# Performance work log

Hardware: AMD Instinct MI355X
Metric: run time of the kernel (lower is better)

## Reference

```python
import jax, jax.numpy as jnp
import numpy as np

D_MODEL = 768
N_HEADS = 12
HEAD_DIM = D_MODEL // N_HEADS


def setup_inputs() -> dict:
    key = jax.random.key(0)
    ks = jax.random.split(key, 9)
    s = 1.0 / np.sqrt(D_MODEL)
    inp = {
        "inputs": jax.random.normal(ks[0], (1, 4096, D_MODEL), dtype=jnp.float32),
        "Wq": jax.random.uniform(ks[1], (D_MODEL, D_MODEL), jnp.float32, -s, s),
        "bq": jax.random.uniform(ks[2], (D_MODEL,), jnp.float32, -s, s),
        "Wk": jax.random.uniform(ks[3], (D_MODEL, D_MODEL), jnp.float32, -s, s),
        "bk": jax.random.uniform(ks[4], (D_MODEL,), jnp.float32, -s, s),
        "Wv": jax.random.uniform(ks[5], (D_MODEL, D_MODEL), jnp.float32, -s, s),
        "bv": jax.random.uniform(ks[6], (D_MODEL,), jnp.float32, -s, s),
        "Wo": jax.random.uniform(ks[7], (D_MODEL, D_MODEL), jnp.float32, -s, s),
        "bo": jax.random.uniform(ks[8], (D_MODEL,), jnp.float32, -s, s),
    }
    return inp


def reference(inputs, Wq, bq, Wk, bk, Wv, bv, Wo, bo):
    B, S, D = inputs.shape
    H, Hd = N_HEADS, HEAD_DIM

    def split_heads(x):  # [B,S,D] -> [B,H,S,Hd]
        return x.reshape(B, S, H, Hd).transpose(0, 2, 1, 3)

    # nn.Linear computes x @ W.T + b
    Q = split_heads(inputs @ Wq.T + bq)
    K = split_heads(inputs @ Wk.T + bk)
    V = split_heads(inputs @ Wv.T + bv)

    scores = jnp.einsum("bhsd,bhtd->bhst", Q, K) / jnp.sqrt(jnp.float32(Hd))
    causal = jnp.tril(jnp.ones((S, S), dtype=bool))  # True = keep
    scores = jnp.where(causal, scores, -jnp.inf)
    attn = jax.nn.softmax(scores, axis=-1)  # dropout is identity in eval

    out = jnp.einsum("bhst,bhtd->bhsd", attn, V)
    out = out.transpose(0, 2, 1, 3).reshape(B, S, D)
    return out @ Wo.T + bo
```

## Files before the change

### kernel.cpp

```cpp
#include <hip/hip_runtime.h>
#include <stdint.h>

#define SEQ 4096
#define DM 768
#define NH 12
#define HD 64

typedef unsigned short u16;
typedef short short8 __attribute__((ext_vector_type(8)));
typedef float floatx4 __attribute__((ext_vector_type(4)));
typedef float floatx16 __attribute__((ext_vector_type(16)));
typedef u16 u16x4 __attribute__((ext_vector_type(4)));

__device__ inline u16 f2b(float f) {
  union { float f; uint32_t u; } v; v.f = f;
  uint32_t u = v.u;
  return (u16)((u + 0x7fffu + ((u >> 16) & 1u)) >> 16);
}

__device__ inline float b2f(u16 x) {
  union { uint32_t u; float f; } v; v.u = ((uint32_t)x) << 16;
  return v.f;
}

#if defined(__has_builtin)
#if __has_builtin(__builtin_amdgcn_cvt_pk_bf16_f32)
#define HAVE_PK_BF16 1
#endif
#endif

__device__ inline uint32_t pk_bf16(float a, float b) {
#ifdef HAVE_PK_BF16
  typedef __bf16 bf16x2_t __attribute__((ext_vector_type(2)));
  union { bf16x2_t v; uint32_t u; } c;
  c.v = __builtin_amdgcn_cvt_pk_bf16_f32(a, b);
  return c.u;
#else
  uint32_t r;
  asm("v_cvt_pk_bf16_f32 %0, %1, %2" : "=v"(r) : "v"(a), "v"(b));
  return r;
#endif
}

__device__ inline void pl32swap(uint32_t& a, uint32_t& b) {
  asm("v_permlane32_swap_b32 %0, %1" : "+v"(a), "+v"(b));
}

__device__ inline void load_lds16(const void* g, void* l) {
  __builtin_amdgcn_global_load_lds(
      (const __attribute__((address_space(1))) uint32_t*)g,
      (__attribute__((address_space(3))) uint32_t*)l, 16, 0, 0);
}

__global__ __launch_bounds__(256) void convert_all(
    const float* __restrict__ X, const float* __restrict__ Wq,
    const float* __restrict__ Wk, const float* __restrict__ Wv,
    const float* __restrict__ Wo,
    u16* __restrict__ Xb, u16* __restrict__ Wqb, u16* __restrict__ Wkb,
    u16* __restrict__ Wvb, u16* __restrict__ Wob) {
  int t = blockIdx.x * 256 + threadIdx.x;
  const int NX = SEQ * DM / 4;
  const int NW = DM * DM / 4;
  const float* src; u16* dst; int off;
  if (t < NX)               { src = X;  dst = Xb;  off = t; }
  else if (t < NX + NW)     { src = Wq; dst = Wqb; off = t - NX; }
  else if (t < NX + 2 * NW) { src = Wk; dst = Wkb; off = t - NX - NW; }
  else if (t < NX + 3 * NW) { src = Wv; dst = Wvb; off = t - NX - 2 * NW; }
  else if (t < NX + 4 * NW) { src = Wo; dst = Wob; off = t - NX - 3 * NW; }
  else return;
  float4 v = *(const float4*)(src + (size_t)off * 4);
  uint2 o;
  o.x = pk_bf16(v.x, v.y);
  o.y = pk_bf16(v.z, v.w);
  *(uint2*)(dst + (size_t)off * 4) = o;
}

__global__ __launch_bounds__(256) void gemm_qkv(
    const u16* __restrict__ Xb,
    const u16* __restrict__ Wqb, const u16* __restrict__ Wkb,
    const u16* __restrict__ Wvb,
    const float* __restrict__ bq, const float* __restrict__ bk,
    const float* __restrict__ bv,
    u16* __restrict__ Qh, u16* __restrict__ Kh, u16* __restrict__ VtG) {
  const u16* W; const float* bias;
  const int z = blockIdx.z;
  if (z == 0)      { W = Wqb; bias = bq; }
  else if (z == 1) { W = Wkb; bias = bk; }
  else             { W = Wvb; bias = bv; }

  __shared__ u16 smem[16384];

  const int tid = threadIdx.x;
  const int wave = tid >> 6, lane = tid & 63;
  const int g = lane >> 4, ln = lane & 15;
  const int m0 = blockIdx.y * 64, n0 = blockIdx.x * 64;
  const int wm = (wave & 1) * 32, wn = (wave >> 1) * 32;
  const int srow = lane >> 3;
  const int schunk = (lane & 7) ^ srow;
  const int swz = ln & 7;

  floatx4 acc[2][2] = {};

#pragma unroll
  for (int i = 0; i < 2; ++i) {
    int u = wave * 2 + i;
    load_lds16(Xb + (size_t)(m0 + u * 8 + srow) * DM + schunk * 8, smem + u * 512);
    load_lds16(W + (size_t)(n0 + u * 8 + srow) * DM + schunk * 8,
               smem + 8192 + u * 512);
  }

  for (int kt = 0; kt < 12; ++kt) {
    const int cur = kt & 1;
    __syncthreads();
    if (kt < 11) {
      const int k0 = (kt + 1) * 64, nb = cur ^ 1;
#pragma unroll
      for (int i = 0; i < 2; ++i) {
        int u = wave * 2 + i;
        load_lds16(Xb + (size_t)(m0 + u * 8 + srow) * DM + k0 + schunk * 8,
                   smem + nb * 4096 + u * 512);
        load_lds16(W + (size_t)(n0 + u * 8 + srow) * DM + k0 + schunk * 8,
                   smem + 8192 + nb * 4096 + u * 512);
      }
    }
    const u16* Ac = smem + cur * 4096;
    const u16* Bc = smem + 8192 + cur * 4096;
    short8 af[2][2], bf[2][2];
#pragma unroll
    for (int mi = 0; mi < 2; ++mi)
#pragma unroll
      for (int kh = 0; kh < 2; ++kh)
        af[mi][kh] = *(const short8*)(Ac + (wm + mi * 16 + ln) * 64 +
                                      ((kh * 4 + g) ^ swz) * 8);
#pragma unroll
    for (int ni = 0; ni < 2; ++ni)
#pragma unroll
      for (int kh = 0; kh < 2; ++kh)
        bf[ni][kh] = *(const short8*)(Bc + (wn + ni * 16 + ln) * 64 +
                                      ((kh * 4 + g) ^ swz) * 8);
#pragma unroll
    for (int kh = 0; kh < 2; ++kh)
#pragma unroll
      for (int mi = 0; mi < 2; ++mi)
#pragma unroll
        for (int ni = 0; ni < 2; ++ni)
          acc[mi][ni] = __builtin_amdgcn_mfma_f32_16x16x32_bf16(
              af[mi][kh], bf[ni][kh], acc[mi][ni], 0, 0, 0);
  }

  const float qscale = 0.125f * 1.44269504089f;
  const int hh = n0 >> 6;
  __syncthreads();

  if (z == 2) {
#pragma unroll
    for (int mi = 0; mi < 2; ++mi) {
      int row0 = wm + mi * 16 + g * 4;
#pragma unroll
      for (int ni = 0; ni < 2; ++ni) {
        int col = wn + ni * 16 + ln;
        float b = bias[n0 + col];
        uint2 o;
        o.x = pk_bf16(acc[mi][ni][0] + b, acc[mi][ni][1] + b);
        o.y = pk_bf16(acc[mi][ni][2] + b, acc[mi][ni][3] + b);
        *(uint2*)(smem + col * 72 + row0) = o;
      }
    }
    __syncthreads();
#pragma unroll
    for (int t = 0; t < 2; ++t) {
      int unit = tid + t * 256;
      int dcol = unit >> 3, ch = unit & 7;
      short8 v = *(const short8*)(smem + dcol * 72 + ch * 8);
      *(short8*)(VtG + ((size_t)(hh * 64 + dcol)) * SEQ + m0 + ch * 8) = v;
    }
  } else {
    u16* out = (z == 0) ? Qh : Kh;
    float cs = (z == 0) ? qscale : 1.0f;
#pragma unroll
    for (int mi = 0; mi < 2; ++mi) {
      int row0 = wm + mi * 16 + g * 4;
#pragma unroll
      for (int ni = 0; ni < 2; ++ni) {
        int col = wn + ni * 16 + ln;
        float b = bias[n0 + col];
        uint32_t w0 = pk_bf16((acc[mi][ni][0] + b) * cs, (acc[mi][ni][1] + b) * cs);
        uint32_t w1 = pk_bf16((acc[mi][ni][2] + b) * cs, (acc[mi][ni][3] + b) * cs);
        smem[(row0 + 0) * 72 + col] = (u16)w0;
        smem[(row0 + 1) * 72 + col] = (u16)(w0 >> 16);
        smem[(row0 + 2) * 72 + col] = (u16)w1;
        smem[(row0 + 3) * 72 + col] = (u16)(w1 >> 16);
      }
    }
    __syncthreads();
#pragma unroll
    for (int t = 0; t < 2; ++t) {
      int unit = tid + t * 256;
      int row = unit >> 3, ch = unit & 7;
      short8 v = *(const short8*)(smem + row * 72 + ch * 8);
      *(short8*)(out + ((size_t)hh * SEQ + m0 + row) * HD + ch * 8) = v;
    }
  }
}

#define CHUNK 16
#define M0 40.0f
__global__ __launch_bounds__(256, 3) void attn_chunk(
    const u16* __restrict__ Qh, const u16* __restrict__ Kh,
    const u16* __restrict__ VtG, u16* __restrict__ Opart,
    float2* __restrict__ Mlp) {
  const int p = blockIdx.y * NH + blockIdx.x;
  const int slot = p % 24, cyc = p / 24;
  const int qq = 3 * (slot & 7) + (slot >> 3);
  const int h = qq >> 1;
  const int b = 79 - (cyc * 2 + (qq & 1));
  int qB, ci;
  if (b < 8)       { qB = b;               ci = 0; }
  else if (b < 24) { int r = b - 8;  qB = 8 + (r >> 1); ci = r & 1; }
  else if (b < 48) { int r = b - 24; int d = r / 3; qB = 16 + d; ci = r - d * 3; }
  else             { int r = b - 48; qB = 24 + (r >> 2); ci = r & 3; }
  const int kb0 = ci * CHUNK;
  const int kb1 = min(kb0 + CHUNK, 2 * qB + 2);

  const int tid = threadIdx.x, wave = tid >> 6, lane = tid & 63;
  const int hi = lane >> 5, lq = lane & 31;
  const int q0 = qB * 128;
  const int qwave = q0 + wave * 32;
  const int srow = lane >> 3;
  const int schunk = (lane & 7) ^ srow;
  const int rsw = lane & 7;

  __shared__ u16 Ks[3 * 4096];
  __shared__ u16 Vt[3 * 4096];

  const int qglob = qwave + lq;
  const u16* Qbase = Qh + ((size_t)h * SEQ + qglob) * HD;
  short8 aq[4];
#pragma unroll
  for (int s = 0; s < 4; ++s)
    aq[s] = *(const short8*)(Qbase + s * 16 + hi * 8);

  floatx16 oacc[2] = {};
  floatx4 lacc = {};

  const size_t kbase = (size_t)h * SEQ * HD;
  const size_t vbase = (size_t)h * 64 * SEQ;

  auto stage = [&](int kbIdx, int buf) {
#pragma unroll
    for (int i = 0; i < 2; ++i) {
      int u = wave * 2 + i;
      load_lds16(Kh + kbase + (size_t)(kbIdx * 64 + u * 8 + srow) * HD + schunk * 8,
                 Ks + buf * 4096 + u * 512);
      load_lds16(VtG + vbase + (size_t)(u * 8 + srow) * SEQ + kbIdx * 64 + schunk * 8,
                 Vt + buf * 4096 + u * 512);
    }
  };

  stage(kb0, 0);
  if (kb0 + 1 < kb1) stage(kb0 + 1, 1);

  for (int kb = kb0; kb < kb1; ++kb) {
    const int cur = (kb - kb0) % 3;
    if (kb + 1 < kb1) asm volatile("s_waitcnt vmcnt(4)" ::: "memory");
    else              asm volatile("s_waitcnt vmcnt(0)" ::: "memory");
    __builtin_amdgcn_s_barrier();
    if (kb + 2 < kb1) stage(kb + 2, (cur + 2) % 3);

    const u16* Kc = Ks + cur * 4096;
    const u16* Vc = Vt + cur * 4096;

    if (kb * 64 > qwave + 31) continue;

    floatx16 st[2];
#pragma unroll
    for (int kblk = 0; kblk < 2; ++kblk)
#pragma unroll
      for (int r = 0; r < 16; ++r) st[kblk][r] = -M0;
    __builtin_amdgcn_s_setprio(1);
#pragma unroll
    for (int s = 0; s < 4; ++s)
#pragma unroll
      for (int kblk = 0; kblk < 2; ++kblk) {
        short8 kf = *(const short8*)(Kc + (kblk * 32 + lq) * 64 +
                                     ((s * 2 + hi) ^ rsw) * 8);
        st[kblk] = __builtin_amdgcn_mfma_f32_32x32x16_bf16(kf, aq[s], st[kblk],
                                                           0, 0, 0);
      }
    __builtin_amdgcn_s_setprio(0);

    if (kb * 64 + 63 > qwave) {
#pragma unroll
      for (int kblk = 0; kblk < 2; ++kblk)
#pragma unroll
        for (int r = 0; r < 16; ++r) {
          int key = kb * 64 + kblk * 32 + (r & 3) + 8 * (r >> 2) + 4 * hi;
          if (key > qglob) st[kblk][r] = -1e30f;
        }
    }

    uint32_t w[2][8];
#pragma unroll
    for (int kblk = 0; kblk < 2; ++kblk) {
#pragma unroll
      for (int r = 0; r < 16; ++r)
        st[kblk][r] = __builtin_amdgcn_exp2f(st[kblk][r]);
#pragma unroll
      for (int r = 0; r < 4; ++r)
        lacc[r] += st[kblk][r] + st[kblk][4 + r] + st[kblk][8 + r] +
                   st[kblk][12 + r];
#pragma unroll
      for (int i = 0; i < 8; ++i)
        w[kblk][i] = pk_bf16(st[kblk][2 * i], st[kblk][2 * i + 1]);
    }

    __builtin_amdgcn_s_setprio(1);
#pragma unroll
    for (int ks = 0; ks < 4; ++ks) {
      const int kblk = ks >> 1, base = (ks & 1) * 4;
      uint32_t d0 = w[kblk][base + 0], d2 = w[kblk][base + 2];
      uint32_t d1 = w[kblk][base + 1], d3 = w[kblk][base + 3];
      pl32swap(d0, d2);
      pl32swap(d1, d3);
      union { uint32_t u[4]; short8 s; } bp;
      bp.u[0] = d0; bp.u[1] = d1; bp.u[2] = d2; bp.u[3] = d3;
#pragma unroll
      for (int dblk = 0; dblk < 2; ++dblk) {
        short8 vf = *(const short8*)(Vc + (dblk * 32 + lq) * 64 +
                                     ((ks * 2 + hi) ^ rsw) * 8);
        oacc[dblk] = __builtin_amdgcn_mfma_f32_32x32x16_bf16(vf, bp.s, oacc[dblk],
                                                             0, 0, 0);
      }
    }
    __builtin_amdgcn_s_setprio(0);
  }

  float l_i = lacc[0] + lacc[1] + lacc[2] + lacc[3];
  l_i += __shfl_xor(l_i, 32);

  const int slot2 = (h * 32 + qB) * 4 + ci;
  float inv = 1.f / l_i;
  int qloc = wave * 32 + lq;
  u16* Op = Opart + (size_t)slot2 * 8192 + qloc * 64;
#pragma unroll
  for (int dblk = 0; dblk < 2; ++dblk)
#pragma unroll
    for (int qd = 0; qd < 4; ++qd) {
      uint2 o;
      o.x = pk_bf16(oacc[dblk][qd * 4 + 0] * inv, oacc[dblk][qd * 4 + 1] * inv);
      o.y = pk_bf16(oacc[dblk][qd * 4 + 2] * inv, oacc[dblk][qd * 4 + 3] * inv);
      *(uint2*)(Op + dblk * 32 + qd * 8 + hi * 4) = o;
    }
  if (hi == 0) Mlp[(size_t)slot2 * 128 + qloc] = make_float2(M0, l_i);
}

__global__ __launch_bounds__(256) void attn_merge(
    const u16* __restrict__ Opart, const float2* __restrict__ Mlp,
    u16* __restrict__ Ob) {
  const int h = blockIdx.x, qB = blockIdx.y;
  const int n = (qB >> 3) + 1;
  const int base = (h * 32 + qB) * 4;
  const int q = threadIdx.x >> 1;
  const int d0 = (threadIdx.x & 1) * 32;

  float m[4], l[4];
  float M = -1e30f;
  for (int i = 0; i < n; ++i) {
    float2 ml = Mlp[(size_t)(base + i) * 128 + q];
    m[i] = ml.x; l[i] = ml.y;
    M = fmaxf(M, m[i]);
  }
  float w[4], L = 0.f;
  for (int i = 0; i < n; ++i) {
    w[i] = l[i] * __builtin_amdgcn_exp2f(m[i] - M);
    L += w[i];
  }
  float invL = 1.f / L;

  float acc[32];
#pragma unroll
  for (int j = 0; j < 32; ++j) acc[j] = 0.f;
  for (int i = 0; i < n; ++i) {
    float wi = w[i] * invL;
    const u16* src = Opart + (size_t)(base + i) * 8192 + q * 64 + d0;
#pragma unroll
    for (int c = 0; c < 4; ++c) {
      short8 a = ((const short8*)src)[c];
#pragma unroll
      for (int j = 0; j < 8; ++j) acc[c * 8 + j] += wi * b2f((u16)a[j]);
    }
  }

  u16* dst = Ob + (size_t)(qB * 128 + q) * DM + h * HD + d0;
#pragma unroll
  for (int c = 0; c < 4; ++c) {
    uint4 o;
    o.x = pk_bf16(acc[c * 8 + 0], acc[c * 8 + 1]);
    o.y = pk_bf16(acc[c * 8 + 2], acc[c * 8 + 3]);
    o.z = pk_bf16(acc[c * 8 + 4], acc[c * 8 + 5]);
    o.w = pk_bf16(acc[c * 8 + 6], acc[c * 8 + 7]);
    ((uint4*)dst)[c] = o;
  }
}

__global__ __launch_bounds__(256) void gemm_out(
    const u16* __restrict__ Ab, const u16* __restrict__ Wob,
    const float* __restrict__ bo, float* __restrict__ Cout) {
  __shared__ u16 smem[16384];

  const int tid = threadIdx.x;
  const int wave = tid >> 6, lane = tid & 63;
  const int g = lane >> 4, ln = lane & 15;
  const int m0 = blockIdx.y * 64, n0 = blockIdx.x * 64;
  const int wm = (wave & 1) * 32, wn = (wave >> 1) * 32;
  const int srow = lane >> 3;
  const int schunk = (lane & 7) ^ srow;
  const int swz = ln & 7;

  floatx4 acc[2][2] = {};

#pragma unroll
  for (int i = 0; i < 2; ++i) {
    int u = wave * 2 + i;
    load_lds16(Ab + (size_t)(m0 + u * 8 + srow) * DM + schunk * 8, smem + u * 512);
    load_lds16(Wob + (size_t)(n0 + u * 8 + srow) * DM + schunk * 8,
               smem + 8192 + u * 512);
  }

  for (int kt = 0; kt < 12; ++kt) {
    const int cur = kt & 1;
    __syncthreads();
    if (kt < 11) {
      const int k0 = (kt + 1) * 64, nb = cur ^ 1;
#pragma unroll
      for (int i = 0; i < 2; ++i) {
        int u = wave * 2 + i;
        load_lds16(Ab + (size_t)(m0 + u * 8 + srow) * DM + k0 + schunk * 8,
                   smem + nb * 4096 + u * 512);
        load_lds16(Wob + (size_t)(n0 + u * 8 + srow) * DM + k0 + schunk * 8,
                   smem + 8192 + nb * 4096 + u * 512);
      }
    }
    const u16* Ac = smem + cur * 4096;
    const u16* Bc = smem + 8192 + cur * 4096;
    short8 af[2][2], bf[2][2];
#pragma unroll
    for (int mi = 0; mi < 2; ++mi)
#pragma unroll
      for (int kh = 0; kh < 2; ++kh)
        af[mi][kh] = *(const short8*)(Ac + (wm + mi * 16 + ln) * 64 +
                                      ((kh * 4 + g) ^ swz) * 8);
#pragma unroll
    for (int ni = 0; ni < 2; ++ni)
#pragma unroll
      for (int kh = 0; kh < 2; ++kh)
        bf[ni][kh] = *(const short8*)(Bc + (wn + ni * 16 + ln) * 64 +
                                      ((kh * 4 + g) ^ swz) * 8);
#pragma unroll
    for (int kh = 0; kh < 2; ++kh)
#pragma unroll
      for (int mi = 0; mi < 2; ++mi)
#pragma unroll
        for (int ni = 0; ni < 2; ++ni)
          acc[mi][ni] = __builtin_amdgcn_mfma_f32_16x16x32_bf16(
              af[mi][kh], bf[ni][kh], acc[mi][ni], 0, 0, 0);
  }

#pragma unroll
  for (int mi = 0; mi < 2; ++mi) {
    int row = m0 + wm + mi * 16 + g * 4;
#pragma unroll
    for (int ni = 0; ni < 2; ++ni) {
      int col = n0 + wn + ni * 16 + ln;
      float b = bo[col];
#pragma unroll
      for (int r = 0; r < 4; ++r)
        Cout[(size_t)(row + r) * DM + col] = acc[mi][ni][r] + b;
    }
  }
}

extern "C" void kernel_launch(void* const* d_in, const int* in_sizes, int n_in,
                              void* d_out, int out_size, void* d_ws, size_t ws_size,
                              hipStream_t stream) {
  const float* X  = (const float*)d_in[0];
  const float* Wq = (const float*)d_in[1];
  const float* bq = (const float*)d_in[2];
  const float* Wk = (const float*)d_in[3];
  const float* bk = (const float*)d_in[4];
  const float* Wv = (const float*)d_in[5];
  const float* bv = (const float*)d_in[6];
  const float* Wo = (const float*)d_in[7];
  const float* bo = (const float*)d_in[8];
  float* out = (float*)d_out;

  char* ws = (char*)d_ws;
  u16* Xb  = (u16*)ws; ws += (size_t)SEQ * DM * 2;
  u16* Wqb = (u16*)ws; ws += (size_t)DM * DM * 2;
  u16* Wkb = (u16*)ws; ws += (size_t)DM * DM * 2;
  u16* Wvb = (u16*)ws; ws += (size_t)DM * DM * 2;
  u16* Wob = (u16*)ws; ws += (size_t)DM * DM * 2;
  u16* Qh  = (u16*)ws; ws += (size_t)NH * SEQ * HD * 2;
  u16* Kh  = (u16*)ws; ws += (size_t)NH * SEQ * HD * 2;
  u16* VtG = (u16*)ws; ws += (size_t)NH * SEQ * HD * 2;
  u16* Ob  = (u16*)ws; ws += (size_t)SEQ * DM * 2;
  u16* Opart = (u16*)ws; ws += (size_t)NH * 32 * 4 * 128 * 64 * 2;
  float2* Mlp = (float2*)ws; ws += (size_t)NH * 32 * 4 * 128 * sizeof(float2);

  convert_all<<<5376, 256, 0, stream>>>(X, Wq, Wk, Wv, Wo, Xb, Wqb, Wkb, Wvb, Wob);

  dim3 gq(DM / 64, SEQ / 64, 3);
  gemm_qkv<<<gq, 256, 0, stream>>>(Xb, Wqb, Wkb, Wvb, bq, bk, bv, Qh, Kh, VtG);

  dim3 ga(NH, 80);
  attn_chunk<<<ga, 256, 0, stream>>>(Qh, Kh, VtG, Opart, Mlp);

  dim3 gm(NH, 32);
  attn_merge<<<gm, 256, 0, stream>>>(Opart, Mlp, Ob);

  dim3 go(DM / 64, SEQ / 64);
  gemm_out<<<go, 256, 0, stream>>>(Ob, Wob, bo, out);
}
```

Before: 176.9 us.

## Split causal attention into smaller key chunks with more blocks and occupancy

Halves the key-chunk size, so the attention grid grows from 80 to 144 block rows per head with a new mapping from block index to (query block, chunk). The pipeline drops from triple to double buffering to cut LDS and raise the occupancy hint from 3 to 5 blocks. Because every chunk uses the same fixed max M0, the merge now stores only the row sum l and skips the max rescaling. The workspace is reorganised so the partial outputs overlay the bf16 input and weight buffers, which are dead after the QKV GEMM. The aim is better load balance and latency hiding, at the cost of more partial outputs to write and merge and less prefetch depth.

```diff
diff --git a/kernel.cpp b/kernel.cpp
--- a/kernel.cpp
+++ b/kernel.cpp
@@ -203,24 +203,30 @@
   }
 }
 
-#define CHUNK 16
+#define CHUNK 8
 #define M0 40.0f
-__global__ __launch_bounds__(256, 3) void attn_chunk(
+__global__ __launch_bounds__(256, 5) void attn_chunk(
     const u16* __restrict__ Qh, const u16* __restrict__ Kh,
     const u16* __restrict__ VtG, u16* __restrict__ Opart,
-    float2* __restrict__ Mlp) {
+    float* __restrict__ Lp) {
   const int p = blockIdx.y * NH + blockIdx.x;
   const int slot = p % 24, cyc = p / 24;
   const int qq = 3 * (slot & 7) + (slot >> 3);
   const int h = qq >> 1;
-  const int b = 79 - (cyc * 2 + (qq & 1));
-  int qB, ci;
-  if (b < 8)       { qB = b;               ci = 0; }
-  else if (b < 24) { int r = b - 8;  qB = 8 + (r >> 1); ci = r & 1; }
-  else if (b < 48) { int r = b - 24; int d = r / 3; qB = 16 + d; ci = r - d * 3; }
-  else             { int r = b - 48; qB = 24 + (r >> 2); ci = r & 3; }
+  const int j = cyc * 2 + (qq & 1);
+  const int r = 143 - j;
+  int g = 0;
+#pragma unroll
+  for (int t = 1; t < 8; ++t)
+    if (2 * t * (t + 1) <= r) g = t;
+  const int gp1 = g + 1;
+  const int rr = r - 2 * g * gp1;
+  const int dq = rr / gp1;
+  const int qB = 4 * g + dq;
+  const int ci = rr - dq * gp1;
   const int kb0 = ci * CHUNK;
   const int kb1 = min(kb0 + CHUNK, 2 * qB + 2);
+  const int slot2 = h * 144 + gp1 * (2 * g + (qB & 3)) + ci;
 
   const int tid = threadIdx.x, wave = tid >> 6, lane = tid & 63;
   const int hi = lane >> 5, lq = lane & 31;
@@ -230,8 +236,8 @@
   const int schunk = (lane & 7) ^ srow;
   const int rsw = lane & 7;
 
-  __shared__ u16 Ks[3 * 4096];
-  __shared__ u16 Vt[3 * 4096];
+  __shared__ u16 Ks[2 * 4096];
+  __shared__ u16 Vt[2 * 4096];
 
   const int qglob = qwave + lq;
   const u16* Qbase = Qh + ((size_t)h * SEQ + qglob) * HD;
@@ -258,14 +264,11 @@
   };
 
   stage(kb0, 0);
-  if (kb0 + 1 < kb1) stage(kb0 + 1, 1);
 
   for (int kb = kb0; kb < kb1; ++kb) {
-    const int cur = (kb - kb0) % 3;
-    if (kb + 1 < kb1) asm volatile("s_waitcnt vmcnt(4)" ::: "memory");
-    else              asm volatile("s_waitcnt vmcnt(0)" ::: "memory");
-    __builtin_amdgcn_s_barrier();
-    if (kb + 2 < kb1) stage(kb + 2, (cur + 2) % 3);
+    const int cur = (kb - kb0) & 1;
+    __syncthreads();
+    if (kb + 1 < kb1) stage(kb + 1, cur ^ 1);
 
     const u16* Kc = Ks + cur * 4096;
     const u16* Vc = Vt + cur * 4096;
@@ -276,7 +279,7 @@
 #pragma unroll
     for (int kblk = 0; kblk < 2; ++kblk)
 #pragma unroll
-      for (int r = 0; r < 16; ++r) st[kblk][r] = -M0;
+      for (int r2 = 0; r2 < 16; ++r2) st[kblk][r2] = -M0;
     __builtin_amdgcn_s_setprio(1);
 #pragma unroll
     for (int s = 0; s < 4; ++s)
@@ -293,9 +296,9 @@
 #pragma unroll
       for (int kblk = 0; kblk < 2; ++kblk)
 #pragma unroll
-        for (int r = 0; r < 16; ++r) {
-          int key = kb * 64 + kblk * 32 + (r & 3) + 8 * (r >> 2) + 4 * hi;
-          if (key > qglob) st[kblk][r] = -1e30f;
+        for (int r2 = 0; r2 < 16; ++r2) {
+          int key = kb * 64 + kblk * 32 + (r2 & 3) + 8 * (r2 >> 2) + 4 * hi;
+          if (key > qglob) st[kblk][r2] = -1e30f;
         }
     }
 
@@ -303,12 +306,12 @@
 #pragma unroll
     for (int kblk = 0; kblk < 2; ++kblk) {
 #pragma unroll
-      for (int r = 0; r < 16; ++r)
-        st[kblk][r] = __builtin_amdgcn_exp2f(st[kblk][r]);
-#pragma unroll
-      for (int r = 0; r < 4; ++r)
-        lacc[r] += st[kblk][r] + st[kblk][4 + r] + st[kblk][8 + r] +
-                   st[kblk][12 + r];
+      for (int r2 = 0; r2 < 16; ++r2)
+        st[kblk][r2] = __builtin_amdgcn_exp2f(st[kblk][r2]);
+#pragma unroll
+      for (int r2 = 0; r2 < 4; ++r2)
+        lacc[r2] += st[kblk][r2] + st[kblk][4 + r2] + st[kblk][8 + r2] +
+                    st[kblk][12 + r2];
 #pragma unroll
       for (int i = 0; i < 8; ++i)
         w[kblk][i] = pk_bf16(st[kblk][2 * i], st[kblk][2 * i + 1]);
@@ -338,7 +341,6 @@
   float l_i = lacc[0] + lacc[1] + lacc[2] + lacc[3];
   l_i += __shfl_xor(l_i, 32);
 
-  const int slot2 = (h * 32 + qB) * 4 + ci;
   float inv = 1.f / l_i;
   int qloc = wave * 32 + lq;
   u16* Op = Opart + (size_t)slot2 * 8192 + qloc * 64;
@@ -351,43 +353,34 @@
       o.y = pk_bf16(oacc[dblk][qd * 4 + 2] * inv, oacc[dblk][qd * 4 + 3] * inv);
       *(uint2*)(Op + dblk * 32 + qd * 8 + hi * 4) = o;
     }
-  if (hi == 0) Mlp[(size_t)slot2 * 128 + qloc] = make_float2(M0, l_i);
+  if (hi == 0) Lp[(size_t)slot2 * 128 + qloc] = l_i;
 }
 
 __global__ __launch_bounds__(256) void attn_merge(
-    const u16* __restrict__ Opart, const float2* __restrict__ Mlp,
+    const u16* __restrict__ Opart, const float* __restrict__ Lp,
     u16* __restrict__ Ob) {
   const int h = blockIdx.x, qB = blockIdx.y;
-  const int n = (qB >> 3) + 1;
-  const int base = (h * 32 + qB) * 4;
+  const int g = qB >> 2;
+  const int n = g + 1;
+  const int base = h * 144 + (g + 1) * (2 * g + (qB & 3));
   const int q = threadIdx.x >> 1;
   const int d0 = (threadIdx.x & 1) * 32;
 
-  float m[4], l[4];
-  float M = -1e30f;
+  float L = 0.f;
+  for (int i = 0; i < n; ++i) L += Lp[(size_t)(base + i) * 128 + q];
+  float invL = 1.f / L;
+
+  float acc[32];
+#pragma unroll
+  for (int jj = 0; jj < 32; ++jj) acc[jj] = 0.f;
   for (int i = 0; i < n; ++i) {
-    float2 ml = Mlp[(size_t)(base + i) * 128 + q];
-    m[i] = ml.x; l[i] = ml.y;
-    M = fmaxf(M, m[i]);
-  }
-  float w[4], L = 0.f;
-  for (int i = 0; i < n; ++i) {
-    w[i] = l[i] * __builtin_amdgcn_exp2f(m[i] - M);
-    L += w[i];
-  }
-  float invL = 1.f / L;
-
-  float acc[32];
-#pragma unroll
-  for (int j = 0; j < 32; ++j) acc[j] = 0.f;
-  for (int i = 0; i < n; ++i) {
-    float wi = w[i] * invL;
+    float wi = Lp[(size_t)(base + i) * 128 + q] * invL;
     const u16* src = Opart + (size_t)(base + i) * 8192 + q * 64 + d0;
 #pragma unroll
     for (int c = 0; c < 4; ++c) {
       short8 a = ((const short8*)src)[c];
 #pragma unroll
-      for (int j = 0; j < 8; ++j) acc[c * 8 + j] += wi * b2f((u16)a[j]);
+      for (int jj = 0; jj < 8; ++jj) acc[c * 8 + jj] += wi * b2f((u16)a[jj]);
     }
   }
 
@@ -495,28 +488,29 @@
   float* out = (float*)d_out;
 
   char* ws = (char*)d_ws;
-  u16* Xb  = (u16*)ws; ws += (size_t)SEQ * DM * 2;
-  u16* Wqb = (u16*)ws; ws += (size_t)DM * DM * 2;
-  u16* Wkb = (u16*)ws; ws += (size_t)DM * DM * 2;
-  u16* Wvb = (u16*)ws; ws += (size_t)DM * DM * 2;
   u16* Wob = (u16*)ws; ws += (size_t)DM * DM * 2;
   u16* Qh  = (u16*)ws; ws += (size_t)NH * SEQ * HD * 2;
   u16* Kh  = (u16*)ws; ws += (size_t)NH * SEQ * HD * 2;
   u16* VtG = (u16*)ws; ws += (size_t)NH * SEQ * HD * 2;
   u16* Ob  = (u16*)ws; ws += (size_t)SEQ * DM * 2;
-  u16* Opart = (u16*)ws; ws += (size_t)NH * 32 * 4 * 128 * 64 * 2;
-  float2* Mlp = (float2*)ws; ws += (size_t)NH * 32 * 4 * 128 * sizeof(float2);
+  float* Lp = (float*)ws; ws += (size_t)NH * 144 * 128 * 4;
+  char* ovl = ws;
+  u16* Xb  = (u16*)ovl;
+  u16* Wqb = Xb + (size_t)SEQ * DM;
+  u16* Wkb = Wqb + (size_t)DM * DM;
+  u16* Wvb = Wkb + (size_t)DM * DM;
+  u16* Opart = (u16*)ovl;
 
   convert_all<<<5376, 256, 0, stream>>>(X, Wq, Wk, Wv, Wo, Xb, Wqb, Wkb, Wvb, Wob);
 
   dim3 gq(DM / 64, SEQ / 64, 3);
   gemm_qkv<<<gq, 256, 0, stream>>>(Xb, Wqb, Wkb, Wvb, bq, bk, bv, Qh, Kh, VtG);
 
-  dim3 ga(NH, 80);
-  attn_chunk<<<ga, 256, 0, stream>>>(Qh, Kh, VtG, Opart, Mlp);
+  dim3 ga(NH, 144);
+  attn_chunk<<<ga, 256, 0, stream>>>(Qh, Kh, VtG, Opart, Lp);
 
   dim3 gm(NH, 32);
-  attn_merge<<<gm, 256, 0, stream>>>(Opart, Mlp, Ob);
+  attn_merge<<<gm, 256, 0, stream>>>(Opart, Lp, Ob);
 
   dim3 go(DM / 64, SEQ / 64);
   gemm_out<<<go, 256, 0, stream>>>(Ob, Wob, bo, out);
```

New measurement: 204.4 us. 15.5% more time.
